# Performance work log

Hardware: AMD Instinct MI355X
Metric: run time of the kernel (lower is better)

Reference implementation:

```python
import jax, jax.numpy as jnp
import numpy as np

N = 4096      # num_nodes
U = 64        # num_units
IN = 2        # input_dim
DIM = U + IN  # 66
H = 4         # attention heads
ALPHA = 0.2   # leaky slope inside attention scores
SLOPE = 0.01  # nn.LeakyReLU() default for subnet activations
NEG_INF = -9e15


def setup_inputs() -> dict:
    key = jax.random.key(0)
    ks = jax.random.split(key, 20)
    def gn(k, shape, fan):
        return jax.random.normal(k, shape, dtype=jnp.float32) / np.float32(np.sqrt(fan))
    adj = jax.random.randint(ks[2], (N, N), 0, 2, dtype=jnp.int32)
    adj = jnp.maximum(adj, jnp.eye(N, dtype=jnp.int32))  # ensure self-loops
    return {
        "inputs": jax.random.normal(ks[0], (1, N * IN), dtype=jnp.float32),
        "hx": jax.random.normal(ks[1], (1, N, U), dtype=jnp.float32),
        "adj": adj,
        "m1_W": gn(ks[3], (H, DIM, DIM), DIM),
        "m1_a1": gn(ks[4], (H, DIM), DIM),
        "m1_a2": gn(ks[5], (H, DIM), DIM),
        "m1_Wout": gn(ks[6], (H * DIM, DIM), H * DIM),
        "m1_ao1": gn(ks[7], (DIM,), DIM),
        "m1_ao2": gn(ks[8], (DIM,), DIM),
        "m2_W": gn(ks[9], (H, DIM, DIM), DIM),
        "m2_a1": gn(ks[10], (H, DIM), DIM),
        "m2_a2": gn(ks[11], (H, DIM), DIM),
        "m2_Wout": gn(ks[12], (H * DIM, DIM), H * DIM),
        "m2_ao1": gn(ks[13], (DIM,), DIM),
        "m2_ao2": gn(ks[14], (DIM,), DIM),
        "g1_W": gn(ks[15], (DIM, 2 * U), DIM),
        "g1_b": jnp.zeros((2 * U,), dtype=jnp.float32),
        "g2_W": gn(ks[16], (DIM, U), DIM),
        "g2_b": jnp.zeros((U,), dtype=jnp.float32),
    }


def gat_layer(x, W, a1, a2, mask):
    # x: [N,Fin], W: [Fin,Fout], a1/a2: [Fout], mask: [N,N] bool
    h = x @ W                                   # [N,Fout]
    f1 = h @ a1                                 # [N] source term
    f2 = h @ a2                                 # [N] target term
    e = jax.nn.leaky_relu(f1[:, None] + f2[None, :], ALPHA)  # [N,N]
    e = jnp.where(mask, e, NEG_INF)
    attn = jax.nn.softmax(e, axis=-1)
    return attn @ h                             # [N,Fout]


def subnet(x, W, a1, a2, Wout, ao1, ao2, mask):
    # multi-head GAT, concat heads, activation, output GAT layer, activation
    heads = jax.vmap(gat_layer, in_axes=(None, 0, 0, 0, None))(x, W, a1, a2, mask)  # [H,N,DIM]
    hcat = jnp.transpose(heads, (1, 0, 2)).reshape(x.shape[0], -1)                   # [N,H*DIM]
    hcat = jax.nn.leaky_relu(hcat, SLOPE)
    out = gat_layer(hcat, Wout, ao1, ao2, mask)                                      # [N,DIM]
    return jax.nn.leaky_relu(out, SLOPE)


def reference(inputs, hx, adj, m1_W, m1_a1, m1_a2, m1_Wout, m1_ao1, m1_ao2,
              m2_W, m2_a1, m2_a2, m2_Wout, m2_ao1, m2_ao2,
              g1_W, g1_b, g2_W, g2_b):
    mask = adj > 0
    xi = inputs.reshape(N, IN)
    xh = hx.reshape(N, U)
    # _GAT1: concat(inputs, hx) -> GATSubNet1 -> linear -> sigmoid -> split r,u
    x1 = jnp.concatenate([xi, xh], axis=-1)                 # [N,DIM]
    g1 = subnet(x1, m1_W, m1_a1, m1_a2, m1_Wout, m1_ao1, m1_ao2, mask)
    value = jax.nn.sigmoid(g1 @ g1_W + g1_b)                # [N,2U]
    r, u = value[:, :U], value[:, U:]
    # _GAT2: concat(inputs, r*hx) -> GATSubNet2 -> linear -> tanh
    x2 = jnp.concatenate([xi, r * xh], axis=-1)             # [N,DIM]
    g2 = subnet(x2, m2_W, m2_a1, m2_a2, m2_Wout, m2_ao1, m2_ao2, mask)
    c = jnp.tanh(g2 @ g2_W + g2_b)                          # [N,U]
    new_state = u * xh + (1.0 - u) * c
    return new_state.reshape(1, N, U)
```

## Files before the change

kernel.cpp:

```cpp
#include <hip/hip_runtime.h>
#include <hip/hip_bf16.h>

constexpr int kN = 4096;
constexpr int kDim = 66;
constexpr int kH = 4;
constexpr int kU = 64;
constexpr float kAlpha = 0.2f;
constexpr float kSlope = 0.01f;
constexpr float kLog2e = 1.44269504f;

typedef _Float16 half8 __attribute__((ext_vector_type(8)));
typedef _Float16 half2t __attribute__((ext_vector_type(2)));
typedef __attribute__((ext_vector_type(4))) float floatx4;

__device__ inline unsigned int fkey(float f){
  unsigned int u = __float_as_uint(f);
  return (u & 0x80000000u) ? ~u : (u | 0x80000000u);
}
__device__ inline float funkey(unsigned int k){
  unsigned int u = (k & 0x80000000u) ? (k ^ 0x80000000u) : ~k;
  return __uint_as_float(u);
}

__device__ __forceinline__ void gld_lds16(const void* g, void* l){
  __builtin_amdgcn_global_load_lds((const __attribute__((address_space(1))) unsigned int*)g,
                                   (__attribute__((address_space(3))) unsigned int*)l, 16, 0, 0);
}

__global__ void setup_k(const int* __restrict__ adj, unsigned long long* __restrict__ packed,
                        const float* __restrict__ in2, const float* __restrict__ hx,
                        _Float16* __restrict__ x1b, _Float16* __restrict__ x2b,
                        const float* __restrict__ m1W, const float* __restrict__ m1a1, const float* __restrict__ m1a2,
                        const float* __restrict__ m1Wo, const float* __restrict__ m1ao1, const float* __restrict__ m1ao2,
                        const float* __restrict__ m2W, const float* __restrict__ m2a1, const float* __restrict__ m2a2,
                        const float* __restrict__ m2Wo, const float* __restrict__ m2ao1, const float* __restrict__ m2ao2,
                        const float* __restrict__ g1W, const float* __restrict__ g1b,
                        const float* __restrict__ g2W, const float* __restrict__ g2b,
                        _Float16* __restrict__ B1t, _Float16* __restrict__ B1t2,
                        _Float16* __restrict__ B2t, _Float16* __restrict__ B2t2,
                        _Float16* __restrict__ Bgt, _Float16* __restrict__ Bft,
                        unsigned int* __restrict__ fmaxbuf){
  int bb = blockIdx.x, t = threadIdx.x;
  if (bb < 16384){
    int gid = bb * 256 + t;
    unsigned long long m = __ballot(adj[gid] != 0);
    if ((t & 63) == 0) packed[gid >> 6] = m;
    return;
  }
  if (bb < 16384 + 1024){
    int i = (bb - 16384) * 4 + (t >> 6);
    int c = t & 63;
    x1b[(size_t)i * 96 + 2 + c] = (_Float16)hx[(size_t)i * kU + c];
    if (c < 2){
      _Float16 xv = (_Float16)in2[i * 2 + c];
      x1b[(size_t)i * 96 + c] = xv;
      x2b[(size_t)i * 96 + c] = xv;
    }
    if (c < 30){
      x1b[(size_t)i * 96 + 66 + c] = (_Float16)0.f;
      x2b[(size_t)i * 96 + 66 + c] = (_Float16)0.f;
    }
    return;
  }
  int b = bb - (16384 + 1024);
  if (b < 8){
    int m = b & 3;
    const float* W  = (b < 4 ? m1W  : m2W)  + (size_t)m * kDim * kDim;
    const float* a1 = (b < 4 ? m1a1 : m2a1) + m * kDim;
    const float* a2 = (b < 4 ? m1a2 : m2a2) + m * kDim;
    _Float16* Bo = (b < 4 ? B1t : B1t2) + (size_t)m * 80 * 96;
    __shared__ float Ws[kDim * kDim];
    __shared__ float wa1s[kDim], wa2s[kDim];
    for (int z = t; z < kDim * kDim; z += 256) Ws[z] = W[z];
    __syncthreads();
    if (t < kDim){
      float s1 = 0.f, s2 = 0.f;
      for (int d = 0; d < kDim; d++){ float wv = Ws[t * kDim + d]; s1 += wv * a1[d]; s2 += wv * a2[d]; }
      wa1s[t] = s1; wa2s[t] = s2;
    }
    __syncthreads();
    for (int z = t; z < 80 * 96; z += 256){
      int nn = z / 96, k = z % 96;
      float val = 0.f;
      if (k < kDim){
        if (nn < kDim) val = Ws[k * kDim + nn];
        else if (nn == 66) val = wa1s[k];
        else if (nn == 67) val = wa2s[k];
      }
      Bo[z] = (_Float16)val;
    }
  } else if (b < 10){
    const float* Wo  = (b == 8 ? m1Wo  : m2Wo);
    const float* ao1 = (b == 8 ? m1ao1 : m2ao1);
    const float* ao2 = (b == 8 ? m1ao2 : m2ao2);
    _Float16* Bo = (b == 8 ? B2t : B2t2);
    __shared__ float wo1s[264], wo2s[264];
    for (int k = t; k < 264; k += 256){
      float s1 = 0.f, s2 = 0.f;
      for (int d = 0; d < kDim; d++){ float wv = Wo[(size_t)k * kDim + d]; s1 += wv * ao1[d]; s2 += wv * ao2[d]; }
      wo1s[k] = s1; wo2s[k] = s2;
    }
    __syncthreads();
    for (int z = t; z < 80 * 288; z += 256){
      int nn = z / 288, k = z % 288;
      int h = k / 72, c = k - h * 72;
      float val = 0.f;
      if (c < 66){
        int kk = h * 66 + c;
        if (nn < kDim) val = Wo[(size_t)kk * kDim + nn];
        else if (nn == 66) val = wo1s[kk];
        else if (nn == 67) val = wo2s[kk];
      }
      Bo[z] = (_Float16)val;
    }
  } else if (b == 10){
    for (int z = t; z < 128 * 96; z += 256){
      int nn = z / 96, k = z % 96;
      float val = 0.f;
      if (k < kDim) val = g1W[k * 128 + nn];
      else if (k == 66) val = g1b[nn];
      Bgt[z] = (_Float16)val;
    }
  } else {
    if (t < 16) fmaxbuf[t] = 0u;
    for (int z = t; z < 64 * 96; z += 256){
      int nn = z / 96, k = z % 96;
      float val = 0.f;
      if (k < kDim) val = g2W[k * 64 + nn];
      else if (k == 66) val = g2b[nn];
      Bft[z] = (_Float16)val;
    }
  }
}

template<int KSTEPS, int NT, int EPI>
__global__ __launch_bounds__(64) void gemm_k(
    const _Float16* __restrict__ A, const _Float16* __restrict__ Bt,
    void* __restrict__ p0, void* __restrict__ p1, void* __restrict__ p2,
    const float* __restrict__ aux, unsigned int* __restrict__ fmaxp)
{
  constexpr int KP = KSTEPS * 32;
  const int m = blockIdx.y;
  const int i0 = blockIdx.x * 16;
  const int lane = threadIdx.x;
  const int q = lane >> 4, n = lane & 15;
  const int arow = i0 + n;
  const _Float16* Ar = A + (size_t)arow * KP;
  const _Float16* Bm = Bt + (size_t)m * (NT * 16) * KP;
  floatx4 acc[NT];
  #pragma unroll
  for (int v = 0; v < NT; v++) acc[v] = (floatx4){0.f, 0.f, 0.f, 0.f};
  #pragma unroll
  for (int ks = 0; ks < KSTEPS; ks++){
    half8 af = *(const half8*)&Ar[ks * 32 + q * 8];
    #pragma unroll
    for (int nt = 0; nt < NT; nt++){
      half8 bf = *(const half8*)&Bm[(size_t)(nt * 16 + n) * KP + ks * 32 + q * 8];
      acc[nt] = __builtin_amdgcn_mfma_f32_16x16x32_f16(af, bf, acc[nt], 0, 0, 0);
    }
  }
  const int ib = i0 + q * 4;
  if constexpr (EPI == 0){
    _Float16* Ht = (_Float16*)p0 + (size_t)m * 68 * kN;
    float* f1 = (float*)p1 + (size_t)m * kN;
    float* f2 = (float*)p2 + (size_t)m * kN;
    float lm = -3e38f;
    #pragma unroll
    for (int nt = 0; nt < NT; nt++){
      int c = nt * 16 + n;
      if (c < kDim){
        union { _Float16 h[4]; uint2 v; } pk;
        pk.h[0] = (_Float16)acc[nt][0]; pk.h[1] = (_Float16)acc[nt][1];
        pk.h[2] = (_Float16)acc[nt][2]; pk.h[3] = (_Float16)acc[nt][3];
        *(uint2*)&Ht[(size_t)c * kN + ib] = pk.v;
      } else if (c == 66){
        float4 fv; fv.x = acc[nt][0] * kLog2e; fv.y = acc[nt][1] * kLog2e;
        fv.z = acc[nt][2] * kLog2e; fv.w = acc[nt][3] * kLog2e;
        *(float4*)&f1[ib] = fv;
        *(uint2*)&Ht[(size_t)66 * kN + ib] = make_uint2(0x3C003C00u, 0x3C003C00u);
      } else if (c == 67){
        float4 fv; fv.x = acc[nt][0] * kLog2e; fv.y = acc[nt][1] * kLog2e;
        fv.z = acc[nt][2] * kLog2e; fv.w = acc[nt][3] * kLog2e;
        *(float4*)&f2[ib] = fv;
        lm = fmaxf(fmaxf(fv.x, fv.y), fmaxf(fv.z, fv.w));
        *(uint2*)&Ht[(size_t)67 * kN + ib] = make_uint2(0u, 0u);
      }
    }
    lm = fmaxf(lm, __shfl_xor(lm, 16));
    lm = fmaxf(lm, __shfl_xor(lm, 32));
    if (lane == 3) atomicMax(&fmaxp[m], fkey(lm));
  } else if constexpr (EPI == 1){
    float* u = (float*)p0;
    _Float16* x2b = (_Float16*)p1;
    #pragma unroll
    for (int nt = 0; nt < NT; nt++){
      int c = nt * 16 + n;
      #pragma unroll
      for (int r = 0; r < 4; r++){
        float v = 1.f / (1.f + __expf(-acc[nt][r]));
        if (c < 64) x2b[(size_t)(ib + r) * 96 + 2 + c] = (_Float16)(v * aux[(size_t)(ib + r) * kU + c]);
        else        u[(size_t)(ib + r) * kU + (c - 64)] = v;
      }
    }
  } else {
    float* outp = (float*)p0;
    const float* u = (const float*)p1;
    #pragma unroll
    for (int nt = 0; nt < NT; nt++){
      int c = nt * 16 + n;
      #pragma unroll
      for (int r = 0; r < 4; r++){
        float cc = tanhf(acc[nt][r]);
        float uv = u[(size_t)(ib + r) * kU + c];
        outp[(size_t)(ib + r) * kU + c] = uv * aux[(size_t)(ib + r) * kU + c] + (1.f - uv) * cc;
      }
    }
  }
}

template<int JSPLIT>
__global__ __launch_bounds__(256, 4) void attn_mfma_k(
    const _Float16* __restrict__ Ht, const float* __restrict__ f1,
    const float* __restrict__ f2, const unsigned int* __restrict__ fmaxu,
    const unsigned long long* __restrict__ packed,
    _Float16* __restrict__ paccb)
{
  constexpr int JR = kN / JSPLIT;
  constexpr int NCH = JR / 128;
  const int m = blockIdx.y, js = blockIdx.z;
  const int i0 = blockIdx.x * 64;
  const int t = threadIdx.x;
  const int w = t >> 6, lane = t & 63, q = lane >> 4, n = lane & 15;
  const int i = i0 + w * 16 + n;
  const _Float16* Hg = Ht + (size_t)m * 68 * kN;
  const float* f2m = f2 + (size_t)m * kN;
  const float f1v = f1[(size_t)m * kN + i];
  const float fmx = funkey(fmaxu[m]);
  const float t0 = f1v + fmx;
  const float S = fmaxf(t0, kAlpha * t0);
  const float A1f = __builtin_amdgcn_exp2f(t0 - S);
  const float A2f = __builtin_amdgcn_exp2f(kAlpha * t0 - S);
  const half2t a1p = { (_Float16)A1f, (_Float16)A1f };
  const half2t a2p = { (_Float16)A2f, (_Float16)A2f };

  __shared__ __align__(16) _Float16 buf[2][68 * 128];
  __shared__ __align__(16) _Float16 Zro[128];
  __shared__ __align__(16) _Float16 B1h[2][128], B2h[2][128];

  for (int z = t; z < 128; z += 256) Zro[z] = (_Float16)0.f;

  const int r4 = q;
  const int cse = n ^ r4;
  const int cso = cse ^ 4;

  const int jbase = js * JR;
  const unsigned long long* prow = packed + (size_t)i * 64;
  const int jj = (w << 5) | (lane & 31);
  const bool blane = (lane & 32) == 0;

#define STAGE_G(PD, CH) do { \
    const _Float16* gB_ = Hg + jbase + (CH) * 128; \
    _Pragma("unroll") \
    for (int kk_ = 0; kk_ < 5; kk_++){ \
      const int k_ = w + kk_ * 4; \
      if (k_ < 17){ \
        const int row_ = k_ * 4 + r4; \
        const int csw_ = (k_ & 1) ? cso : cse; \
        gld_lds16(gB_ + (size_t)row_ * kN + csw_ * 8, &buf[(PD)][k_ * 512]); \
      } \
    } \
  } while (0)

  floatx4 acc[5];
  #pragma unroll
  for (int v = 0; v < 5; v++) acc[v] = (floatx4){0.f, 0.f, 0.f, 0.f};

  if (blane){
    const float v_ = f2m[jbase + jj] - fmx;
    B1h[0][jj] = (_Float16)__builtin_amdgcn_exp2f(v_);
    B2h[0][jj] = (_Float16)__builtin_amdgcn_exp2f(kAlpha * v_);
  }
  STAGE_G(0, 0);
  __syncthreads();

  int ch = 0;
#define BODY(P) do { \
    const int j0_ = jbase + ch * 128; \
    float f2v_ = 0.f; \
    const bool doB_ = (ch + 1 < NCH) && blane; \
    if (doB_) f2v_ = f2m[j0_ + 128 + jj]; \
    const unsigned long long w0_ = prow[j0_ >> 6]; \
    const unsigned long long w1_ = prow[(j0_ >> 6) + 1]; \
    __builtin_amdgcn_sched_barrier(0); \
    if (ch + 1 < NCH) STAGE_G((P) ^ 1, ch + 1); \
    __builtin_amdgcn_sched_barrier(0); \
    if (doB_){ \
      const float v_ = f2v_ - fmx; \
      B1h[(P) ^ 1][jj] = (_Float16)__builtin_amdgcn_exp2f(v_); \
      B2h[(P) ^ 1][jj] = (_Float16)__builtin_amdgcn_exp2f(kAlpha * v_); \
    } \
    const _Float16* bz_ = (n < 4) ? &buf[(P)][(64 + n) * 128] : Zro; \
    _Pragma("unroll") \
    for (int ks = 0; ks < 4; ks++){ \
      const unsigned long long wsel = (ks < 2) ? w0_ : w1_; \
      const unsigned int bits = (unsigned int)((wsel >> ((ks & 1) * 32 + q * 8)) & 0xffull); \
      union { uint4 v; unsigned int u[4]; } b1v, b2v; \
      b1v.v = *(const uint4*)&B1h[(P)][ks * 32 + q * 8]; \
      b2v.v = *(const uint4*)&B2h[(P)][ks * 32 + q * 8]; \
      union { half8 s; unsigned int u[4]; } af; \
      _Pragma("unroll") \
      for (int e = 0; e < 4; e++){ \
        half2t x1 = __builtin_bit_cast(half2t, b1v.u[e]); \
        half2t x2 = __builtin_bit_cast(half2t, b2v.u[e]); \
        half2t m1 = x1 * a1p; \
        half2t m2 = x2 * a2p; \
        half2t pm = __builtin_elementwise_max(m1, m2); \
        unsigned int mm = (((bits >> (2 * e)) & 1u) ? 0x0000FFFFu : 0u) \
                        | (((bits >> (2 * e + 1)) & 1u) ? 0xFFFF0000u : 0u); \
        af.u[e] = __builtin_bit_cast(unsigned int, pm) & mm; \
      } \
      const int cs_ = ((ks * 4 + q) ^ (n & 7)) * 8; \
      _Pragma("unroll") \
      for (int nt = 0; nt < 4; nt++){ \
        const half8 bf = *(const half8*)&buf[(P)][(nt * 16 + n) * 128 + cs_]; \
        acc[nt] = __builtin_amdgcn_mfma_f32_16x16x32_f16(af.s, bf, acc[nt], 0, 0, 0); \
      } \
      { const half8 bf4 = *(const half8*)&bz_[cs_]; \
        acc[4] = __builtin_amdgcn_mfma_f32_16x16x32_f16(af.s, bf4, acc[4], 0, 0, 0); } \
    } \
    ch++; \
    if (ch < NCH) __syncthreads(); \
  } while (0)

  #pragma unroll 1
  for (int it = 0; it < NCH / 2; it++){
    BODY(0);
    BODY(1);
  }
#undef BODY
#undef STAGE_G

  _Float16* pw = paccb + ((size_t)(m * JSPLIT + js) * kN + (i0 + w * 16)) * 80;
  #pragma unroll
  for (int nt = 0; nt < 5; nt++){
    if (nt < 4 || n < 4){
      #pragma unroll
      for (int r = 0; r < 4; r++)
        pw[(q * 4 + r) * 80 + nt * 16 + n] = (_Float16)acc[nt][r];
    }
  }
}

template<int JSPLIT>
__global__ __launch_bounds__(256) void combine_k(const _Float16* __restrict__ paccb,
                          _Float16* __restrict__ outb,
                          int ostride, int headoff, int ones_col){
  const int m = blockIdx.y;
  const int t = threadIdx.x;
  const int ri = t >> 3, cg = t & 7;
  const int lane = t & 63;
  const int i = blockIdx.x * 32 + ri;
  const _Float16* pb = paccb + ((size_t)m * JSPLIT * kN + i) * 80;
  float accv[2][8];
  #pragma unroll
  for (int k = 0; k < 2; k++)
    #pragma unroll
    for (int e = 0; e < 8; e++) accv[k][e] = 0.f;
  #pragma unroll
  for (int s = 0; s < JSPLIT; s++){
    const _Float16* ps = pb + (size_t)s * kN * 80;
    union { uint4 v; _Float16 h[8]; } uu;
    uu.v = *(const uint4*)&ps[cg * 8];
    #pragma unroll
    for (int e = 0; e < 8; e++) accv[0][e] += (float)uu.h[e];
    if (cg == 0){
      uu.v = *(const uint4*)&ps[64];
      #pragma unroll
      for (int e = 0; e < 8; e++) accv[1][e] += (float)uu.h[e];
    }
  }
  float l = accv[1][2];
  l = __shfl(l, lane & 56, 64);
  const float inv = 1.f / l;
  _Float16* orow = outb + (size_t)i * ostride + m * headoff;
  {
    union { uint4 v; _Float16 h[8]; } uu;
    #pragma unroll
    for (int e = 0; e < 8; e++){
      float v = accv[0][e] * inv;
      v = fmaxf(v, kSlope * v);
      uu.h[e] = (_Float16)v;
    }
    *(uint4*)&orow[cg * 8] = uu.v;
  }
  if (cg == 0){
    union { uint4 v; _Float16 h[8]; } uu;
    #pragma unroll
    for (int e = 0; e < 2; e++){
      float v = accv[1][e] * inv;
      v = fmaxf(v, kSlope * v);
      uu.h[e] = (_Float16)v;
    }
    uu.h[2] = (_Float16)(ones_col ? 1.f : 0.f);
    #pragma unroll
    for (int e = 3; e < 8; e++) uu.h[e] = (_Float16)0.f;
    *(uint4*)&orow[64] = uu.v;
  }
}

extern "C" void kernel_launch(void* const* d_in, const int* in_sizes, int n_in,
                              void* d_out, int out_size, void* d_ws, size_t ws_size,
                              hipStream_t stream){
  const float* inputs  = (const float*)d_in[0];
  const float* hx      = (const float*)d_in[1];
  const int*   adj     = (const int*)d_in[2];
  const float* m1_W    = (const float*)d_in[3];
  const float* m1_a1   = (const float*)d_in[4];
  const float* m1_a2   = (const float*)d_in[5];
  const float* m1_Wout = (const float*)d_in[6];
  const float* m1_ao1  = (const float*)d_in[7];
  const float* m1_ao2  = (const float*)d_in[8];
  const float* m2_W    = (const float*)d_in[9];
  const float* m2_a1   = (const float*)d_in[10];
  const float* m2_a2   = (const float*)d_in[11];
  const float* m2_Wout = (const float*)d_in[12];
  const float* m2_ao1  = (const float*)d_in[13];
  const float* m2_ao2  = (const float*)d_in[14];
  const float* g1_W    = (const float*)d_in[15];
  const float* g1_b    = (const float*)d_in[16];
  const float* g2_W    = (const float*)d_in[17];
  const float* g2_b    = (const float*)d_in[18];
  float* out = (float*)d_out;

  char* ws = (char*)d_ws;
  size_t off = 0;
  auto alloc = [&](size_t bytes) -> void* {
    void* p = ws + off;
    off = (off + bytes + 255) & ~(size_t)255;
    return p;
  };
  unsigned long long* packed = (unsigned long long*)alloc((size_t)kN * 64 * 8);
  _Float16* x1b  = (_Float16*)alloc((size_t)kN * 96 * 2);
  _Float16* x2b  = (_Float16*)alloc((size_t)kN * 96 * 2);
  _Float16* Ht   = (_Float16*)alloc((size_t)kH * 68 * kN * 2);
  _Float16* Hto  = (_Float16*)alloc((size_t)68 * kN * 2);
  _Float16* hcatb= (_Float16*)alloc((size_t)kN * 288 * 2);
  _Float16* gb   = (_Float16*)alloc((size_t)kN * 96 * 2);
  _Float16* g2bv = (_Float16*)alloc((size_t)kN * 96 * 2);
  float* f1   = (float*)alloc((size_t)kH * kN * 4);
  float* f2   = (float*)alloc((size_t)kH * kN * 4);
  float* fo1  = (float*)alloc((size_t)kN * 4);
  float* fo2  = (float*)alloc((size_t)kN * 4);
  unsigned int* fmaxbuf = (unsigned int*)alloc(64);
  float* u    = (float*)alloc((size_t)kN * kU * 4);
  _Float16* paccb = (_Float16*)alloc((size_t)16 * kN * 80 * 2);
  _Float16* B1t  = (_Float16*)alloc((size_t)kH * 80 * 96 * 2);
  _Float16* B1t2 = (_Float16*)alloc((size_t)kH * 80 * 96 * 2);
  _Float16* B2t  = (_Float16*)alloc((size_t)80 * 288 * 2);
  _Float16* B2t2 = (_Float16*)alloc((size_t)80 * 288 * 2);
  _Float16* Bgt  = (_Float16*)alloc((size_t)128 * 96 * 2);
  _Float16* Bft  = (_Float16*)alloc((size_t)64 * 96 * 2);
  (void)ws_size; (void)in_sizes; (void)n_in; (void)out_size;

  setup_k<<<16384 + 1024 + 12, 256, 0, stream>>>(adj, packed, inputs, hx, x1b, x2b,
      m1_W, m1_a1, m1_a2, m1_Wout, m1_ao1, m1_ao2,
      m2_W, m2_a1, m2_a2, m2_Wout, m2_ao1, m2_ao2,
      g1_W, g1_b, g2_W, g2_b,
      B1t, B1t2, B2t, B2t2, Bgt, Bft, fmaxbuf);

  gemm_k<3, 5, 0><<<dim3(256, kH), 64, 0, stream>>>(x1b, B1t, Ht, f1, f2, nullptr, fmaxbuf + 0);
  attn_mfma_k<4><<<dim3(64, kH, 4), 256, 0, stream>>>(Ht, f1, f2, fmaxbuf + 0, packed, paccb);
  combine_k<4><<<dim3(128, kH), 256, 0, stream>>>(paccb, hcatb, 288, 72, 0);
  gemm_k<9, 5, 0><<<dim3(256, 1), 64, 0, stream>>>(hcatb, B2t, Hto, fo1, fo2, nullptr, fmaxbuf + 4);
  attn_mfma_k<16><<<dim3(64, 1, 16), 256, 0, stream>>>(Hto, fo1, fo2, fmaxbuf + 4, packed, paccb);
  combine_k<16><<<dim3(128, 1), 256, 0, stream>>>(paccb, gb, 96, 0, 1);
  gemm_k<3, 8, 1><<<dim3(256, 1), 64, 0, stream>>>(gb, Bgt, u, x2b, nullptr, hx, nullptr);

  gemm_k<3, 5, 0><<<dim3(256, kH), 64, 0, stream>>>(x2b, B1t2, Ht, f1, f2, nullptr, fmaxbuf + 5);
  attn_mfma_k<4><<<dim3(64, kH, 4), 256, 0, stream>>>(Ht, f1, f2, fmaxbuf + 5, packed, paccb);
  combine_k<4><<<dim3(128, kH), 256, 0, stream>>>(paccb, hcatb, 288, 72, 0);
  gemm_k<9, 5, 0><<<dim3(256, 1), 64, 0, stream>>>(hcatb, B2t2, Hto, fo1, fo2, nullptr, fmaxbuf + 9);
  attn_mfma_k<16><<<dim3(64, 1, 16), 256, 0, stream>>>(Hto, fo1, fo2, fmaxbuf + 9, packed, paccb);
  combine_k<16><<<dim3(128, 1), 256, 0, stream>>>(paccb, g2bv, 96, 0, 1);
  gemm_k<3, 4, 2><<<dim3(256, 1), 64, 0, stream>>>(g2bv, Bft, out, u, nullptr, hx, nullptr);
}
```

Baseline: 305.9 us.

## Widen GEMM blocks to four waves, split output columns, reduce output-layer attention split

The small GEMM kernels move from one-wave blocks of 16 rows to 256-thread blocks of 64 rows. The output-layer and gate GEMMs are also split across output-column slabs on a second grid dimension, with the B2 weight buffer padded to 96 rows so each slab reads in-bounds data. The output-layer attention drops from a 16-way to an 8-way J split, and its combine step changes to match. The aim is better occupancy balance and fewer partial-accumulator writes and combines, at the cost of less parallelism in the output attention and more register work per block.

```diff
diff --git a/kernel.cpp b/kernel.cpp
--- a/kernel.cpp
+++ b/kernel.cpp
@@ -101,17 +101,17 @@
       wo1s[k] = s1; wo2s[k] = s2;
     }
     __syncthreads();
-    for (int z = t; z < 80 * 288; z += 256){
+    for (int z = t; z < 96 * 288; z += 256){
       int nn = z / 288, k = z % 288;
       int h = k / 72, c = k - h * 72;
       float val = 0.f;
-      if (c < 66){
+      if (c < 66 && nn < 80){
         int kk = h * 66 + c;
         if (nn < kDim) val = Wo[(size_t)kk * kDim + nn];
         else if (nn == 66) val = wo1s[kk];
         else if (nn == 67) val = wo2s[kk];
       }
-      Bo[z] = (_Float16)val;
+      Bo[(size_t)nn * 288 + k] = (_Float16)val;
     }
   } else if (b == 10){
     for (int z = t; z < 128 * 96; z += 256){
@@ -133,20 +133,22 @@
   }
 }
 
-template<int KSTEPS, int NT, int EPI>
-__global__ __launch_bounds__(64) void gemm_k(
+template<int KSTEPS, int NT, int EPI, bool SLAB>
+__global__ __launch_bounds__(256) void gemm_k(
     const _Float16* __restrict__ A, const _Float16* __restrict__ Bt,
     void* __restrict__ p0, void* __restrict__ p1, void* __restrict__ p2,
     const float* __restrict__ aux, unsigned int* __restrict__ fmaxp)
 {
   constexpr int KP = KSTEPS * 32;
   const int m = blockIdx.y;
-  const int i0 = blockIdx.x * 16;
-  const int lane = threadIdx.x;
-  const int q = lane >> 4, n = lane & 15;
-  const int arow = i0 + n;
+  const int i0 = blockIdx.x * 64;
+  const int t = threadIdx.x;
+  const int w = t >> 6, lane = t & 63, q = lane >> 4, n = lane & 15;
+  const int arow = i0 + w * 16 + n;
   const _Float16* Ar = A + (size_t)arow * KP;
   const _Float16* Bm = Bt + (size_t)m * (NT * 16) * KP;
+  const int head = SLAB ? 0 : m;
+  const int cbase = SLAB ? m * (NT * 16) : 0;
   floatx4 acc[NT];
   #pragma unroll
   for (int v = 0; v < NT; v++) acc[v] = (floatx4){0.f, 0.f, 0.f, 0.f};
@@ -159,15 +161,15 @@
       acc[nt] = __builtin_amdgcn_mfma_f32_16x16x32_f16(af, bf, acc[nt], 0, 0, 0);
     }
   }
-  const int ib = i0 + q * 4;
+  const int ib = i0 + w * 16 + q * 4;
   if constexpr (EPI == 0){
-    _Float16* Ht = (_Float16*)p0 + (size_t)m * 68 * kN;
-    float* f1 = (float*)p1 + (size_t)m * kN;
-    float* f2 = (float*)p2 + (size_t)m * kN;
+    _Float16* Ht = (_Float16*)p0 + (size_t)head * 68 * kN;
+    float* f1 = (float*)p1 + (size_t)head * kN;
+    float* f2 = (float*)p2 + (size_t)head * kN;
     float lm = -3e38f;
     #pragma unroll
     for (int nt = 0; nt < NT; nt++){
-      int c = nt * 16 + n;
+      int c = cbase + nt * 16 + n;
       if (c < kDim){
         union { _Float16 h[4]; uint2 v; } pk;
         pk.h[0] = (_Float16)acc[nt][0]; pk.h[1] = (_Float16)acc[nt][1];
@@ -188,13 +190,13 @@
     }
     lm = fmaxf(lm, __shfl_xor(lm, 16));
     lm = fmaxf(lm, __shfl_xor(lm, 32));
-    if (lane == 3) atomicMax(&fmaxp[m], fkey(lm));
+    if (lane == 3) atomicMax(&fmaxp[head], fkey(lm));
   } else if constexpr (EPI == 1){
     float* u = (float*)p0;
     _Float16* x2b = (_Float16*)p1;
     #pragma unroll
     for (int nt = 0; nt < NT; nt++){
-      int c = nt * 16 + n;
+      int c = cbase + nt * 16 + n;
       #pragma unroll
       for (int r = 0; r < 4; r++){
         float v = 1.f / (1.f + __expf(-acc[nt][r]));
@@ -207,7 +209,7 @@
     const float* u = (const float*)p1;
     #pragma unroll
     for (int nt = 0; nt < NT; nt++){
-      int c = nt * 16 + n;
+      int c = cbase + nt * 16 + n;
       #pragma unroll
       for (int r = 0; r < 4; r++){
         float cc = tanhf(acc[nt][r]);
@@ -456,8 +458,8 @@
   _Float16* paccb = (_Float16*)alloc((size_t)16 * kN * 80 * 2);
   _Float16* B1t  = (_Float16*)alloc((size_t)kH * 80 * 96 * 2);
   _Float16* B1t2 = (_Float16*)alloc((size_t)kH * 80 * 96 * 2);
-  _Float16* B2t  = (_Float16*)alloc((size_t)80 * 288 * 2);
-  _Float16* B2t2 = (_Float16*)alloc((size_t)80 * 288 * 2);
+  _Float16* B2t  = (_Float16*)alloc((size_t)96 * 288 * 2);
+  _Float16* B2t2 = (_Float16*)alloc((size_t)96 * 288 * 2);
   _Float16* Bgt  = (_Float16*)alloc((size_t)128 * 96 * 2);
   _Float16* Bft  = (_Float16*)alloc((size_t)64 * 96 * 2);
   (void)ws_size; (void)in_sizes; (void)n_in; (void)out_size;
@@ -468,19 +470,19 @@
       g1_W, g1_b, g2_W, g2_b,
       B1t, B1t2, B2t, B2t2, Bgt, Bft, fmaxbuf);
 
-  gemm_k<3, 5, 0><<<dim3(256, kH), 64, 0, stream>>>(x1b, B1t, Ht, f1, f2, nullptr, fmaxbuf + 0);
+  gemm_k<3, 5, 0, false><<<dim3(64, kH), 256, 0, stream>>>(x1b, B1t, Ht, f1, f2, nullptr, fmaxbuf + 0);
   attn_mfma_k<4><<<dim3(64, kH, 4), 256, 0, stream>>>(Ht, f1, f2, fmaxbuf + 0, packed, paccb);
   combine_k<4><<<dim3(128, kH), 256, 0, stream>>>(paccb, hcatb, 288, 72, 0);
-  gemm_k<9, 5, 0><<<dim3(256, 1), 64, 0, stream>>>(hcatb, B2t, Hto, fo1, fo2, nullptr, fmaxbuf + 4);
-  attn_mfma_k<16><<<dim3(64, 1, 16), 256, 0, stream>>>(Hto, fo1, fo2, fmaxbuf + 4, packed, paccb);
-  combine_k<16><<<dim3(128, 1), 256, 0, stream>>>(paccb, gb, 96, 0, 1);
-  gemm_k<3, 8, 1><<<dim3(256, 1), 64, 0, stream>>>(gb, Bgt, u, x2b, nullptr, hx, nullptr);
-
-  gemm_k<3, 5, 0><<<dim3(256, kH), 64, 0, stream>>>(x2b, B1t2, Ht, f1, f2, nullptr, fmaxbuf + 5);
+  gemm_k<9, 3, 0, true><<<dim3(64, 2), 256, 0, stream>>>(hcatb, B2t, Hto, fo1, fo2, nullptr, fmaxbuf + 4);
+  attn_mfma_k<8><<<dim3(64, 1, 8), 256, 0, stream>>>(Hto, fo1, fo2, fmaxbuf + 4, packed, paccb);
+  combine_k<8><<<dim3(128, 1), 256, 0, stream>>>(paccb, gb, 96, 0, 1);
+  gemm_k<3, 4, 1, true><<<dim3(64, 2), 256, 0, stream>>>(gb, Bgt, u, x2b, nullptr, hx, nullptr);
+
+  gemm_k<3, 5, 0, false><<<dim3(64, kH), 256, 0, stream>>>(x2b, B1t2, Ht, f1, f2, nullptr, fmaxbuf + 5);
   attn_mfma_k<4><<<dim3(64, kH, 4), 256, 0, stream>>>(Ht, f1, f2, fmaxbuf + 5, packed, paccb);
   combine_k<4><<<dim3(128, kH), 256, 0, stream>>>(paccb, hcatb, 288, 72, 0);
-  gemm_k<9, 5, 0><<<dim3(256, 1), 64, 0, stream>>>(hcatb, B2t2, Hto, fo1, fo2, nullptr, fmaxbuf + 9);
-  attn_mfma_k<16><<<dim3(64, 1, 16), 256, 0, stream>>>(Hto, fo1, fo2, fmaxbuf + 9, packed, paccb);
-  combine_k<16><<<dim3(128, 1), 256, 0, stream>>>(paccb, g2bv, 96, 0, 1);
-  gemm_k<3, 4, 2><<<dim3(256, 1), 64, 0, stream>>>(g2bv, Bft, out, u, nullptr, hx, nullptr);
-}
+  gemm_k<9, 3, 0, true><<<dim3(64, 2), 256, 0, stream>>>(hcatb, B2t2, Hto, fo1, fo2, nullptr, fmaxbuf + 9);
+  attn_mfma_k<8><<<dim3(64, 1, 8), 256, 0, stream>>>(Hto, fo1, fo2, fmaxbuf + 9, packed, paccb);
+  combine_k<8><<<dim3(128, 1), 256, 0, stream>>>(paccb, g2bv, 96, 0, 1);
+  gemm_k<3, 2, 2, true><<<dim3(64, 2), 256, 0, stream>>>(g2bv, Bft, out, u, nullptr, hx, nullptr);
+}
```

Result: no change. 301.2 us (-1.5%).
